# Performance work log

Measured on AMD Instinct MI355X. Metric: run time of the kernel, lower is better.

## Reference

```python
import jax, jax.numpy as jnp
import numpy as np

NMS_SIGMA = 2.0
MASK_THRESH = 0.5
N = 500
H = W = 256
NUM_CLS = 80


def setup_inputs() -> dict:
    key = jax.random.key(0)
    k1, k2, k3 = jax.random.split(key, 3)
    mask_preds = jax.random.uniform(k1, (N, H, W), dtype=jnp.float32)
    cate_scores = jax.random.uniform(k2, (N,), dtype=jnp.float32)
    cate_labels = jax.random.randint(k3, (N,), 0, NUM_CLS, dtype=jnp.int32)
    return {"mask_preds": mask_preds, "cate_scores": cate_scores, "cate_labels": cate_labels}


def reference(mask_preds, cate_scores, cate_labels):
    n = mask_preds.shape[0]
    # binarize masks (SOLOv2 inference: seg_masks = seg_preds > mask_thresh)
    seg_masks = (mask_preds > MASK_THRESH).astype(mask_preds.dtype)  # [N,H,W]
    sum_masks = seg_masks.sum(axis=(1, 2))                           # [N]
    # mask scoring: average soft score inside the binary mask
    seg_scores = (mask_preds * seg_masks).sum(axis=(1, 2)) / jnp.maximum(sum_masks, 1.0)
    scores = cate_scores * seg_scores                                # [N]
    # sort descending by score (matrix-NMS assumes sorted order)
    order = jnp.argsort(-scores)
    scores = scores[order]
    labels = cate_labels[order]
    flat = seg_masks[order].reshape(n, -1)                           # [N,HW]
    sums = sum_masks[order]
    # pairwise mask IoU, upper-triangular (j suppressed by i<j)
    inter = flat @ flat.T                                            # [N,N]
    union = sums[:, None] + sums[None, :] - inter
    iou = jnp.triu(inter / jnp.maximum(union, 1.0), k=1)
    label_match = jnp.triu((labels[:, None] == labels[None, :]).astype(iou.dtype), k=1)
    decay_iou = iou * label_match                                    # [N,N]
    # gaussian matrix-NMS decay
    compensate_iou = decay_iou.max(axis=0)                           # [N]
    decay_matrix = jnp.exp(-NMS_SIGMA * (decay_iou ** 2 - compensate_iou[:, None] ** 2))
    coeff = decay_matrix.min(axis=0)                                 # [N]
    updated_scores = scores * coeff
    return updated_scores
```

## Files before the change

### kernel.cpp

```cpp
#include <hip/hip_runtime.h>
#include <cstdint>

typedef unsigned long long u64;

#define THRESH 0.5f
#define SIGMA 2.0f

#define TPB 64
#define NSPLIT 8
#define CH 64
#define CST 66

__global__ __launch_bounds__(256) void k_pack_score(
    const float* __restrict__ preds, u64* __restrict__ packed,
    double* __restrict__ pssum, int* __restrict__ pcnt, int HW)
{
    const int b = blockIdx.x;
    const int i = b >> 2, sub = b & 3;
    const int seg = HW >> 2;
    const float* src = preds + (size_t)i * HW + (size_t)sub * seg;
    u64* dst = packed + (size_t)i * (HW >> 6) + (size_t)sub * (seg >> 6);
    const int tid = threadIdx.x;
    const int wave = tid >> 6, lane = tid & 63;
    double ssum = 0.0;
    int cnt = 0;
    const int iters = seg >> 10;
    for (int k = 0; k < iters; ++k) {
        const int p = (k << 10) + (wave << 8) + (lane << 2);
        const float4 v = *reinterpret_cast<const float4*>(src + p);
        const bool b0 = v.x > THRESH, b1 = v.y > THRESH, b2 = v.z > THRESH, b3 = v.w > THRESH;
        const u64 m0 = __ballot(b0);
        const u64 m1 = __ballot(b1);
        const u64 m2 = __ballot(b2);
        const u64 m3 = __ballot(b3);
        if (lane < 4) {
            const u64 m = (lane == 0) ? m0 : (lane == 1) ? m1 : (lane == 2) ? m2 : m3;
            dst[(k << 4) + (wave << 2) + lane] = m;
        }
        cnt += (int)b0 + (int)b1 + (int)b2 + (int)b3;
        ssum += (b0 ? (double)v.x : 0.0) + (b1 ? (double)v.y : 0.0)
              + (b2 ? (double)v.z : 0.0) + (b3 ? (double)v.w : 0.0);
    }
    for (int off = 32; off > 0; off >>= 1) {
        ssum += __shfl_down(ssum, off);
        cnt  += __shfl_down(cnt, off);
    }
    __shared__ double ls[4];
    __shared__ int lc[4];
    if (lane == 0) { ls[wave] = ssum; lc[wave] = cnt; }
    __syncthreads();
    if (tid == 0) {
        pssum[b] = ls[0] + ls[1] + ls[2] + ls[3];
        pcnt[b]  = lc[0] + lc[1] + lc[2] + lc[3];
    }
}

__global__ __launch_bounds__(512) void k_sort(
    const double* __restrict__ pssum, const int* __restrict__ pcnt,
    const float* __restrict__ cate, const int* __restrict__ labels,
    float* __restrict__ sScore, float* __restrict__ sSum,
    int* __restrict__ sLabel, int* __restrict__ order, int N)
{
    __shared__ float sc[512];
    const int i = threadIdx.x;
    float si = 0.f, su = 0.f;
    if (i < N) {
        const double S = pssum[4*i] + pssum[4*i+1] + pssum[4*i+2] + pssum[4*i+3];
        const int C = pcnt[4*i] + pcnt[4*i+1] + pcnt[4*i+2] + pcnt[4*i+3];
        si = cate[i] * (float)(S / (double)(C > 1 ? C : 1));
        su = (float)C;
        sc[i] = si;
    }
    __syncthreads();
    if (i < N) {
        int r = 0;
        for (int j = 0; j < N; ++j) {
            const float sj = sc[j];
            r += (sj > si) || (sj == si && j < i);
        }
        order[r] = i;
        sScore[r] = si;
        sSum[r] = su;
        sLabel[r] = labels[i];
    }
}

__global__ __launch_bounds__(256) void k_inter(
    const u64* __restrict__ packed, const int* __restrict__ order,
    unsigned* __restrict__ interBuf, int N, int WORDS, int NT)
{
    __shared__ u64 sm[2 * TPB][CST];
    int b = blockIdx.x;
    int ti = 0, rowlen = NT;
    while (b >= rowlen) { b -= rowlen; ++ti; --rowlen; }
    const int tj = ti + b;
    const int kwords = WORDS / NSPLIT;
    const int kbase = blockIdx.y * kwords;

    const int tid = threadIdx.x;
    const int a = tid >> 4, bb = tid & 15;

    unsigned acc[4][4] = {};
    for (int c = 0; c < kwords / CH; ++c) {
        const int base = kbase + c * CH;
        for (int idx = tid; idx < 2 * TPB * (CH / 2); idx += 256) {
            const int ml = idx >> 5;
            const int w = (idx & 31) << 1;
            const int g = (ml < TPB) ? (ti * TPB + ml) : (tj * TPB + (ml - TPB));
            u64 x0 = 0, x1 = 0;
            if (g < N) {
                const u64* p = packed + (size_t)order[g] * WORDS + base + w;
                x0 = p[0];
                x1 = p[1];
            }
            sm[ml][w] = x0;
            sm[ml][w + 1] = x1;
        }
        __syncthreads();
        #pragma unroll 2
        for (int w = 0; w < CH; w += 2) {
            u64 pi0[4], pi1[4], pj0[4], pj1[4];
            #pragma unroll
            for (int t = 0; t < 4; ++t) { pi0[t] = sm[4*a + t][w]; pi1[t] = sm[4*a + t][w + 1]; }
            #pragma unroll
            for (int s = 0; s < 4; ++s) { pj0[s] = sm[TPB + 4*bb + s][w]; pj1[s] = sm[TPB + 4*bb + s][w + 1]; }
            #pragma unroll
            for (int t = 0; t < 4; ++t)
                #pragma unroll
                for (int s = 0; s < 4; ++s)
                    acc[t][s] += (unsigned)__popcll(pi0[t] & pj0[s])
                               + (unsigned)__popcll(pi1[t] & pj1[s]);
        }
        __syncthreads();
    }
    #pragma unroll
    for (int t = 0; t < 4; ++t)
        #pragma unroll
        for (int s = 0; s < 4; ++s) {
            const int gi = ti * TPB + 4*a + t;
            const int gj = tj * TPB + 4*bb + s;
            if (gj < N && gi < gj) atomicAdd(&interBuf[(size_t)gi * N + gj], acc[t][s]);
        }
}

__global__ __launch_bounds__(256) void k_comp(
    const unsigned* __restrict__ interBuf, const float* __restrict__ sSum,
    const int* __restrict__ sLabel, float* __restrict__ comp, int N)
{
    const int c = blockIdx.x;
    const int tid = threadIdx.x;
    const float suc = sSum[c];
    const int lc_ = sLabel[c];
    float m = 0.0f;
    for (int k = tid; k < c; k += 256) {
        if (sLabel[k] == lc_) {
            const float inter = (float)interBuf[(size_t)k * N + c];
            const float un = sSum[k] + suc - inter;
            m = fmaxf(m, inter / fmaxf(un, 1.0f));
        }
    }
    for (int off = 32; off > 0; off >>= 1) m = fmaxf(m, __shfl_down(m, off));
    __shared__ float lm[4];
    const int wave = tid >> 6, lane = tid & 63;
    if (lane == 0) lm[wave] = m;
    __syncthreads();
    if (tid == 0) comp[c] = fmaxf(fmaxf(lm[0], lm[1]), fmaxf(lm[2], lm[3]));
}

__global__ __launch_bounds__(256) void k_final(
    const unsigned* __restrict__ interBuf, const float* __restrict__ comp,
    const float* __restrict__ sSum, const int* __restrict__ sLabel,
    const float* __restrict__ sScore, float* __restrict__ out, int N)
{
    const int j = blockIdx.x;
    const int tid = threadIdx.x;
    const float suj = sSum[j];
    const int lj = sLabel[j];
    float m = -3.0e38f;
    for (int i = tid; i < N; i += 256) {
        const float ci = comp[i];
        float d = 0.0f;
        if (i < j && sLabel[i] == lj) {
            const float inter = (float)interBuf[(size_t)i * N + j];
            const float un = sSum[i] + suj - inter;
            d = inter / fmaxf(un, 1.0f);
        }
        m = fmaxf(m, d * d - ci * ci);
    }
    for (int off = 32; off > 0; off >>= 1) m = fmaxf(m, __shfl_down(m, off));
    __shared__ float lm[4];
    const int wave = tid >> 6, lane = tid & 63;
    if (lane == 0) lm[wave] = m;
    __syncthreads();
    if (tid == 0) {
        const float mm = fmaxf(fmaxf(lm[0], lm[1]), fmaxf(lm[2], lm[3]));
        out[j] = sScore[j] * expf(-SIGMA * mm);
    }
}

extern "C" void kernel_launch(void* const* d_in, const int* in_sizes, int n_in,
                              void* d_out, int out_size, void* d_ws, size_t ws_size,
                              hipStream_t stream)
{
    const float* preds  = (const float*)d_in[0];
    const float* cate   = (const float*)d_in[1];
    const int*   labels = (const int*)d_in[2];
    float* out = (float*)d_out;

    const int N = in_sizes[1];
    const int HW = in_sizes[0] / N;
    const int WORDS = HW >> 6;

    char* ws = (char*)d_ws;
    size_t off = 0;
    auto take = [&](size_t bytes) -> void* {
        void* p = ws + off;
        off = (off + bytes + 255) & ~(size_t)255;
        return p;
    };
    u64*      packed   = (u64*)     take((size_t)N * WORDS * sizeof(u64));
    double*   pssum    = (double*)  take((size_t)N * 4 * sizeof(double));
    int*      pcnt     = (int*)     take((size_t)N * 4 * sizeof(int));
    float*    sScore   = (float*)   take((size_t)N * sizeof(float));
    float*    sSum     = (float*)   take((size_t)N * sizeof(float));
    int*      sLabel   = (int*)     take((size_t)N * sizeof(int));
    int*      order    = (int*)     take((size_t)N * sizeof(int));
    float*    comp     = (float*)   take((size_t)N * sizeof(float));
    unsigned* interBuf = (unsigned*)take((size_t)N * N * sizeof(unsigned));
    (void)ws_size; (void)n_in; (void)out_size;

    hipMemsetAsync(interBuf, 0, (size_t)N * N * sizeof(unsigned), stream);

    k_pack_score<<<N * 4, 256, 0, stream>>>(preds, packed, pssum, pcnt, HW);

    k_sort<<<1, 512, 0, stream>>>(pssum, pcnt, cate, labels,
                                  sScore, sSum, sLabel, order, N);

    const int NT = (N + TPB - 1) / TPB;
    dim3 grid(NT * (NT + 1) / 2, NSPLIT);
    k_inter<<<grid, 256, 0, stream>>>(packed, order, interBuf, N, WORDS, NT);

    k_comp<<<N, 256, 0, stream>>>(interBuf, sSum, sLabel, comp, N);

    k_final<<<N, 256, 0, stream>>>(interBuf, comp, sSum, sLabel, sScore, out, N);
}
```

Before: 278.2 us.

## Fuse pipeline into one cooperative persistent kernel with grid syncs

Merges the pack, sort, intersection, compensation and final kernels into a single cooperative kernel that separates the stages with grid-wide syncs and uses a union for shared memory. The memset and atomic adds are replaced by per-split partial intersection counts that the later stages sum, and the packing loop is unrolled by two. The aim is to remove launch gaps, the memset and atomic contention. In exchange, grid.sync has its own cost, the grid size is capped by occupancy, and the partial-count buffer is eight times larger to read.

After: 449.4 us. +61.5%, slower.

```diff
diff --git a/kernel.cpp b/kernel.cpp
--- a/kernel.cpp
+++ b/kernel.cpp
@@ -1,200 +1,210 @@
 #include <hip/hip_runtime.h>
+#include <hip/hip_cooperative_groups.h>
 #include <cstdint>
 
+namespace cg = cooperative_groups;
 typedef unsigned long long u64;
 
 #define THRESH 0.5f
 #define SIGMA 2.0f
-
 #define TPB 64
 #define NSPLIT 8
 #define CH 64
 #define CST 66
 
-__global__ __launch_bounds__(256) void k_pack_score(
-    const float* __restrict__ preds, u64* __restrict__ packed,
-    double* __restrict__ pssum, int* __restrict__ pcnt, int HW)
+union SharedU {
+    u64 sm[2 * TPB][CST];
+    struct { double ls[4]; int lc[4]; } red;
+    float lmx[4];
+};
+
+__global__ __launch_bounds__(256, 2) void k_mega(
+    const float* __restrict__ preds, const float* __restrict__ cate,
+    const int* __restrict__ labels,
+    u64* __restrict__ packed, double* __restrict__ pssum, int* __restrict__ pcnt,
+    float* __restrict__ scoreBuf, float* __restrict__ sumBuf,
+    float* __restrict__ sScore, float* __restrict__ sSum,
+    int* __restrict__ sLabel, int* __restrict__ order,
+    float* __restrict__ comp, unsigned* __restrict__ part8,
+    float* __restrict__ out, int N, int HW)
 {
-    const int b = blockIdx.x;
-    const int i = b >> 2, sub = b & 3;
-    const int seg = HW >> 2;
-    const float* src = preds + (size_t)i * HW + (size_t)sub * seg;
-    u64* dst = packed + (size_t)i * (HW >> 6) + (size_t)sub * (seg >> 6);
+    cg::grid_group grid = cg::this_grid();
+    __shared__ SharedU sh;
     const int tid = threadIdx.x;
     const int wave = tid >> 6, lane = tid & 63;
-    double ssum = 0.0;
-    int cnt = 0;
-    const int iters = seg >> 10;
-    for (int k = 0; k < iters; ++k) {
-        const int p = (k << 10) + (wave << 8) + (lane << 2);
-        const float4 v = *reinterpret_cast<const float4*>(src + p);
-        const bool b0 = v.x > THRESH, b1 = v.y > THRESH, b2 = v.z > THRESH, b3 = v.w > THRESH;
-        const u64 m0 = __ballot(b0);
-        const u64 m1 = __ballot(b1);
-        const u64 m2 = __ballot(b2);
-        const u64 m3 = __ballot(b3);
-        if (lane < 4) {
-            const u64 m = (lane == 0) ? m0 : (lane == 1) ? m1 : (lane == 2) ? m2 : m3;
-            dst[(k << 4) + (wave << 2) + lane] = m;
-        }
-        cnt += (int)b0 + (int)b1 + (int)b2 + (int)b3;
-        ssum += (b0 ? (double)v.x : 0.0) + (b1 ? (double)v.y : 0.0)
-              + (b2 ? (double)v.z : 0.0) + (b3 ? (double)v.w : 0.0);
-    }
-    for (int off = 32; off > 0; off >>= 1) {
-        ssum += __shfl_down(ssum, off);
-        cnt  += __shfl_down(cnt, off);
-    }
-    __shared__ double ls[4];
-    __shared__ int lc[4];
-    if (lane == 0) { ls[wave] = ssum; lc[wave] = cnt; }
-    __syncthreads();
-    if (tid == 0) {
-        pssum[b] = ls[0] + ls[1] + ls[2] + ls[3];
-        pcnt[b]  = lc[0] + lc[1] + lc[2] + lc[3];
-    }
-}
-
-__global__ __launch_bounds__(512) void k_sort(
-    const double* __restrict__ pssum, const int* __restrict__ pcnt,
-    const float* __restrict__ cate, const int* __restrict__ labels,
-    float* __restrict__ sScore, float* __restrict__ sSum,
-    int* __restrict__ sLabel, int* __restrict__ order, int N)
-{
-    __shared__ float sc[512];
-    const int i = threadIdx.x;
-    float si = 0.f, su = 0.f;
-    if (i < N) {
+    const int WORDS = HW >> 6;
+
+    {
+        const int seg = HW >> 2;
+        const int iters = seg >> 10;
+        for (int task = blockIdx.x; task < N * 4; task += gridDim.x) {
+            const int i = task >> 2, sub = task & 3;
+            const float* src = preds + (size_t)i * HW + (size_t)sub * seg;
+            u64* dst = packed + (size_t)i * WORDS + (size_t)sub * (seg >> 6);
+            double ssum = 0.0;
+            int cnt = 0;
+            for (int k = 0; k < iters; k += 2) {
+                const int p0 = (k << 10) + (wave << 8) + (lane << 2);
+                const float4 v0 = *reinterpret_cast<const float4*>(src + p0);
+                const float4 v1 = *reinterpret_cast<const float4*>(src + p0 + 1024);
+                const bool a0 = v0.x > THRESH, a1 = v0.y > THRESH, a2 = v0.z > THRESH, a3 = v0.w > THRESH;
+                const bool b0 = v1.x > THRESH, b1 = v1.y > THRESH, b2 = v1.z > THRESH, b3 = v1.w > THRESH;
+                const u64 ma0 = __ballot(a0), ma1 = __ballot(a1), ma2 = __ballot(a2), ma3 = __ballot(a3);
+                const u64 mb0 = __ballot(b0), mb1 = __ballot(b1), mb2 = __ballot(b2), mb3 = __ballot(b3);
+                if (lane < 4) {
+                    const u64 ma = (lane == 0) ? ma0 : (lane == 1) ? ma1 : (lane == 2) ? ma2 : ma3;
+                    const u64 mb = (lane == 0) ? mb0 : (lane == 1) ? mb1 : (lane == 2) ? mb2 : mb3;
+                    dst[(k << 4) + (wave << 2) + lane] = ma;
+                    dst[((k + 1) << 4) + (wave << 2) + lane] = mb;
+                }
+                cnt += (int)a0 + (int)a1 + (int)a2 + (int)a3
+                     + (int)b0 + (int)b1 + (int)b2 + (int)b3;
+                ssum += (a0 ? (double)v0.x : 0.0) + (a1 ? (double)v0.y : 0.0)
+                      + (a2 ? (double)v0.z : 0.0) + (a3 ? (double)v0.w : 0.0)
+                      + (b0 ? (double)v1.x : 0.0) + (b1 ? (double)v1.y : 0.0)
+                      + (b2 ? (double)v1.z : 0.0) + (b3 ? (double)v1.w : 0.0);
+            }
+            for (int off = 32; off > 0; off >>= 1) {
+                ssum += __shfl_down(ssum, off);
+                cnt  += __shfl_down(cnt, off);
+            }
+            if (lane == 0) { sh.red.ls[wave] = ssum; sh.red.lc[wave] = cnt; }
+            __syncthreads();
+            if (tid == 0) {
+                pssum[task] = sh.red.ls[0] + sh.red.ls[1] + sh.red.ls[2] + sh.red.ls[3];
+                pcnt[task]  = sh.red.lc[0] + sh.red.lc[1] + sh.red.lc[2] + sh.red.lc[3];
+            }
+            __syncthreads();
+        }
+    }
+    grid.sync();
+
+    for (int i = blockIdx.x * 256 + tid; i < N; i += gridDim.x * 256) {
         const double S = pssum[4*i] + pssum[4*i+1] + pssum[4*i+2] + pssum[4*i+3];
         const int C = pcnt[4*i] + pcnt[4*i+1] + pcnt[4*i+2] + pcnt[4*i+3];
-        si = cate[i] * (float)(S / (double)(C > 1 ? C : 1));
-        su = (float)C;
-        sc[i] = si;
-    }
-    __syncthreads();
-    if (i < N) {
+        scoreBuf[i] = cate[i] * (float)(S / (double)(C > 1 ? C : 1));
+        sumBuf[i] = (float)C;
+    }
+    grid.sync();
+
+    for (int i = blockIdx.x * 256 + tid; i < N; i += gridDim.x * 256) {
+        const float si = scoreBuf[i];
         int r = 0;
         for (int j = 0; j < N; ++j) {
-            const float sj = sc[j];
+            const float sj = scoreBuf[j];
             r += (sj > si) || (sj == si && j < i);
         }
         order[r] = i;
         sScore[r] = si;
-        sSum[r] = su;
+        sSum[r] = sumBuf[i];
         sLabel[r] = labels[i];
     }
-}
-
-__global__ __launch_bounds__(256) void k_inter(
-    const u64* __restrict__ packed, const int* __restrict__ order,
-    unsigned* __restrict__ interBuf, int N, int WORDS, int NT)
-{
-    __shared__ u64 sm[2 * TPB][CST];
-    int b = blockIdx.x;
-    int ti = 0, rowlen = NT;
-    while (b >= rowlen) { b -= rowlen; ++ti; --rowlen; }
-    const int tj = ti + b;
-    const int kwords = WORDS / NSPLIT;
-    const int kbase = blockIdx.y * kwords;
-
-    const int tid = threadIdx.x;
-    const int a = tid >> 4, bb = tid & 15;
-
-    unsigned acc[4][4] = {};
-    for (int c = 0; c < kwords / CH; ++c) {
-        const int base = kbase + c * CH;
-        for (int idx = tid; idx < 2 * TPB * (CH / 2); idx += 256) {
-            const int ml = idx >> 5;
-            const int w = (idx & 31) << 1;
-            const int g = (ml < TPB) ? (ti * TPB + ml) : (tj * TPB + (ml - TPB));
-            u64 x0 = 0, x1 = 0;
-            if (g < N) {
-                const u64* p = packed + (size_t)order[g] * WORDS + base + w;
-                x0 = p[0];
-                x1 = p[1];
-            }
-            sm[ml][w] = x0;
-            sm[ml][w + 1] = x1;
-        }
-        __syncthreads();
-        #pragma unroll 2
-        for (int w = 0; w < CH; w += 2) {
-            u64 pi0[4], pi1[4], pj0[4], pj1[4];
-            #pragma unroll
-            for (int t = 0; t < 4; ++t) { pi0[t] = sm[4*a + t][w]; pi1[t] = sm[4*a + t][w + 1]; }
-            #pragma unroll
-            for (int s = 0; s < 4; ++s) { pj0[s] = sm[TPB + 4*bb + s][w]; pj1[s] = sm[TPB + 4*bb + s][w + 1]; }
+    grid.sync();
+
+    {
+        const int NT = (N + TPB - 1) / TPB;
+        const int ntri = NT * (NT + 1) / 2;
+        const int kwords = WORDS / NSPLIT;
+        const int a = tid >> 4, bb = tid & 15;
+        for (int task = blockIdx.x; task < ntri * NSPLIT; task += gridDim.x) {
+            const int split = task / ntri;
+            int b = task - split * ntri;
+            int ti = 0, rowlen = NT;
+            while (b >= rowlen) { b -= rowlen; ++ti; --rowlen; }
+            const int tj = ti + b;
+            const int kbase = split * kwords;
+
+            unsigned acc[4][4] = {};
+            for (int c = 0; c < kwords / CH; ++c) {
+                const int base = kbase + c * CH;
+                for (int idx = tid; idx < 2 * TPB * (CH / 2); idx += 256) {
+                    const int ml = idx >> 5;
+                    const int w = (idx & 31) << 1;
+                    const int g = (ml < TPB) ? (ti * TPB + ml) : (tj * TPB + (ml - TPB));
+                    u64 x0 = 0, x1 = 0;
+                    if (g < N) {
+                        const u64* p = packed + (size_t)order[g] * WORDS + base + w;
+                        x0 = p[0];
+                        x1 = p[1];
+                    }
+                    sh.sm[ml][w] = x0;
+                    sh.sm[ml][w + 1] = x1;
+                }
+                __syncthreads();
+                #pragma unroll 2
+                for (int w = 0; w < CH; w += 2) {
+                    u64 pi0[4], pi1[4], pj0[4], pj1[4];
+                    #pragma unroll
+                    for (int t = 0; t < 4; ++t) { pi0[t] = sh.sm[4*a + t][w]; pi1[t] = sh.sm[4*a + t][w + 1]; }
+                    #pragma unroll
+                    for (int s = 0; s < 4; ++s) { pj0[s] = sh.sm[TPB + 4*bb + s][w]; pj1[s] = sh.sm[TPB + 4*bb + s][w + 1]; }
+                    #pragma unroll
+                    for (int t = 0; t < 4; ++t)
+                        #pragma unroll
+                        for (int s = 0; s < 4; ++s)
+                            acc[t][s] += (unsigned)__popcll(pi0[t] & pj0[s])
+                                       + (unsigned)__popcll(pi1[t] & pj1[s]);
+                }
+                __syncthreads();
+            }
             #pragma unroll
             for (int t = 0; t < 4; ++t)
                 #pragma unroll
-                for (int s = 0; s < 4; ++s)
-                    acc[t][s] += (unsigned)__popcll(pi0[t] & pj0[s])
-                               + (unsigned)__popcll(pi1[t] & pj1[s]);
-        }
-        __syncthreads();
-    }
-    #pragma unroll
-    for (int t = 0; t < 4; ++t)
-        #pragma unroll
-        for (int s = 0; s < 4; ++s) {
-            const int gi = ti * TPB + 4*a + t;
-            const int gj = tj * TPB + 4*bb + s;
-            if (gj < N && gi < gj) atomicAdd(&interBuf[(size_t)gi * N + gj], acc[t][s]);
-        }
-}
-
-__global__ __launch_bounds__(256) void k_comp(
-    const unsigned* __restrict__ interBuf, const float* __restrict__ sSum,
-    const int* __restrict__ sLabel, float* __restrict__ comp, int N)
-{
-    const int c = blockIdx.x;
-    const int tid = threadIdx.x;
-    const float suc = sSum[c];
-    const int lc_ = sLabel[c];
-    float m = 0.0f;
-    for (int k = tid; k < c; k += 256) {
-        if (sLabel[k] == lc_) {
-            const float inter = (float)interBuf[(size_t)k * N + c];
-            const float un = sSum[k] + suc - inter;
-            m = fmaxf(m, inter / fmaxf(un, 1.0f));
-        }
-    }
-    for (int off = 32; off > 0; off >>= 1) m = fmaxf(m, __shfl_down(m, off));
-    __shared__ float lm[4];
-    const int wave = tid >> 6, lane = tid & 63;
-    if (lane == 0) lm[wave] = m;
-    __syncthreads();
-    if (tid == 0) comp[c] = fmaxf(fmaxf(lm[0], lm[1]), fmaxf(lm[2], lm[3]));
-}
-
-__global__ __launch_bounds__(256) void k_final(
-    const unsigned* __restrict__ interBuf, const float* __restrict__ comp,
-    const float* __restrict__ sSum, const int* __restrict__ sLabel,
-    const float* __restrict__ sScore, float* __restrict__ out, int N)
-{
-    const int j = blockIdx.x;
-    const int tid = threadIdx.x;
-    const float suj = sSum[j];
-    const int lj = sLabel[j];
-    float m = -3.0e38f;
-    for (int i = tid; i < N; i += 256) {
-        const float ci = comp[i];
-        float d = 0.0f;
-        if (i < j && sLabel[i] == lj) {
-            const float inter = (float)interBuf[(size_t)i * N + j];
-            const float un = sSum[i] + suj - inter;
-            d = inter / fmaxf(un, 1.0f);
-        }
-        m = fmaxf(m, d * d - ci * ci);
-    }
-    for (int off = 32; off > 0; off >>= 1) m = fmaxf(m, __shfl_down(m, off));
-    __shared__ float lm[4];
-    const int wave = tid >> 6, lane = tid & 63;
-    if (lane == 0) lm[wave] = m;
-    __syncthreads();
-    if (tid == 0) {
-        const float mm = fmaxf(fmaxf(lm[0], lm[1]), fmaxf(lm[2], lm[3]));
-        out[j] = sScore[j] * expf(-SIGMA * mm);
+                for (int s = 0; s < 4; ++s) {
+                    const int gi = ti * TPB + 4*a + t;
+                    const int gj = tj * TPB + 4*bb + s;
+                    if (gj < N && gi < gj)
+                        part8[((size_t)gi * N + gj) * NSPLIT + split] = acc[t][s];
+                }
+        }
+    }
+    grid.sync();
+
+    for (int c = blockIdx.x; c < N; c += gridDim.x) {
+        const float suc = sSum[c];
+        const int lc_ = sLabel[c];
+        float m = 0.0f;
+        for (int k = tid; k < c; k += 256) {
+            if (sLabel[k] == lc_) {
+                const uint4* p = reinterpret_cast<const uint4*>(part8 + ((size_t)k * N + c) * NSPLIT);
+                const uint4 q0 = p[0], q1 = p[1];
+                const float inter = (float)(q0.x + q0.y + q0.z + q0.w + q1.x + q1.y + q1.z + q1.w);
+                const float un = sSum[k] + suc - inter;
+                m = fmaxf(m, inter / fmaxf(un, 1.0f));
+            }
+        }
+        for (int off = 32; off > 0; off >>= 1) m = fmaxf(m, __shfl_down(m, off));
+        if (lane == 0) sh.lmx[wave] = m;
+        __syncthreads();
+        if (tid == 0) comp[c] = fmaxf(fmaxf(sh.lmx[0], sh.lmx[1]), fmaxf(sh.lmx[2], sh.lmx[3]));
+        __syncthreads();
+    }
+    grid.sync();
+
+    for (int j = blockIdx.x; j < N; j += gridDim.x) {
+        const float suj = sSum[j];
+        const int lj = sLabel[j];
+        float m = -3.0e38f;
+        for (int i = tid; i < N; i += 256) {
+            const float ci = comp[i];
+            float d = 0.0f;
+            if (i < j && sLabel[i] == lj) {
+                const uint4* p = reinterpret_cast<const uint4*>(part8 + ((size_t)i * N + j) * NSPLIT);
+                const uint4 q0 = p[0], q1 = p[1];
+                const float inter = (float)(q0.x + q0.y + q0.z + q0.w + q1.x + q1.y + q1.z + q1.w);
+                const float un = sSum[i] + suj - inter;
+                d = inter / fmaxf(un, 1.0f);
+            }
+            m = fmaxf(m, d * d - ci * ci);
+        }
+        for (int off = 32; off > 0; off >>= 1) m = fmaxf(m, __shfl_down(m, off));
+        if (lane == 0) sh.lmx[wave] = m;
+        __syncthreads();
+        if (tid == 0) {
+            const float mm = fmaxf(fmaxf(sh.lmx[0], sh.lmx[1]), fmaxf(sh.lmx[2], sh.lmx[3]));
+            out[j] = sScore[j] * expf(-SIGMA * mm);
+        }
+        __syncthreads();
     }
 }
 
@@ -207,8 +217,8 @@
     const int*   labels = (const int*)d_in[2];
     float* out = (float*)d_out;
 
-    const int N = in_sizes[1];
-    const int HW = in_sizes[0] / N;
+    int N = in_sizes[1];
+    int HW = in_sizes[0] / N;
     const int WORDS = HW >> 6;
 
     char* ws = (char*)d_ws;
@@ -221,26 +231,28 @@
     u64*      packed   = (u64*)     take((size_t)N * WORDS * sizeof(u64));
     double*   pssum    = (double*)  take((size_t)N * 4 * sizeof(double));
     int*      pcnt     = (int*)     take((size_t)N * 4 * sizeof(int));
+    float*    scoreBuf = (float*)   take((size_t)N * sizeof(float));
+    float*    sumBuf   = (float*)   take((size_t)N * sizeof(float));
     float*    sScore   = (float*)   take((size_t)N * sizeof(float));
     float*    sSum     = (float*)   take((size_t)N * sizeof(float));
     int*      sLabel   = (int*)     take((size_t)N * sizeof(int));
     int*      order    = (int*)     take((size_t)N * sizeof(int));
     float*    comp     = (float*)   take((size_t)N * sizeof(float));
-    unsigned* interBuf = (unsigned*)take((size_t)N * N * sizeof(unsigned));
+    unsigned* part8    = (unsigned*)take((size_t)N * N * NSPLIT * sizeof(unsigned));
     (void)ws_size; (void)n_in; (void)out_size;
 
-    hipMemsetAsync(interBuf, 0, (size_t)N * N * sizeof(unsigned), stream);
-
-    k_pack_score<<<N * 4, 256, 0, stream>>>(preds, packed, pssum, pcnt, HW);
-
-    k_sort<<<1, 512, 0, stream>>>(pssum, pcnt, cate, labels,
-                                  sScore, sSum, sLabel, order, N);
-
-    const int NT = (N + TPB - 1) / TPB;
-    dim3 grid(NT * (NT + 1) / 2, NSPLIT);
-    k_inter<<<grid, 256, 0, stream>>>(packed, order, interBuf, N, WORDS, NT);
-
-    k_comp<<<N, 256, 0, stream>>>(interBuf, sSum, sLabel, comp, N);
-
-    k_final<<<N, 256, 0, stream>>>(interBuf, comp, sSum, sLabel, sScore, out, N);
+    int occ = 0;
+    if (hipOccupancyMaxActiveBlocksPerMultiprocessor(&occ, k_mega, 256, 0) != hipSuccess || occ < 1)
+        occ = 2;
+    int gridBlocks = occ * 256;
+    if (gridBlocks > 2048) gridBlocks = 2048;
+
+    void* args[] = {
+        (void*)&preds, (void*)&cate, (void*)&labels,
+        (void*)&packed, (void*)&pssum, (void*)&pcnt,
+        (void*)&scoreBuf, (void*)&sumBuf,
+        (void*)&sScore, (void*)&sSum, (void*)&sLabel, (void*)&order,
+        (void*)&comp, (void*)&part8, (void*)&out, (void*)&N, (void*)&HW
+    };
+    hipLaunchCooperativeKernel(k_mega, dim3(gridBlocks), dim3(256), args, 0, stream);
 }
```
